# Kernel optimization log

Hardware: AMD Instinct MI355X
Metric: run time of the kernel (lower is better)

## Reference

```python
import jax, jax.numpy as jnp
import numpy as np


def setup_inputs() -> dict:
    key = jax.random.key(0)
    k1, k2, k3 = jax.random.split(key, 3)
    B, T, N = 2, 16, 128
    INP, COND, OUT = 64, 64, 128
    x = jax.random.normal(k1, (B, T, N, INP), dtype=jnp.float32)
    cond = jax.random.normal(k2, (B, N, N, COND), dtype=jnp.float32)
    in_dim = 6 * INP + 2 * COND  # 512
    W = jax.random.normal(k3, (in_dim, OUT), dtype=jnp.float32) / np.sqrt(in_dim)
    b = jnp.zeros((OUT,), dtype=jnp.float32)
    return {"x": x, "cond": cond, "W": W, "b": b}


def reference(x, cond, W, b):
    # x: (B,T,N,C), cond: (B,N,N,Cc), W: (6C+2Cc, O), b: (O,)
    B, T, N, C = x.shape
    Cc = cond.shape[-1]
    # temporal boundary-zeroed copies (faithful to torch cat of zeros + slices)
    x1 = x.at[:, 0].set(0.0)        # zeros at t=0
    x2 = x.at[:, -1].set(0.0)       # zeros at t=T-1
    xc = jnp.concatenate([x1, x, x2], axis=-1)  # (B,T,N,3C)
    # decompose the big linear over the concat [x1_pair, x2_pair, cond1, cond2]
    W1 = W[: 3 * C]
    W2 = W[3 * C: 6 * C]
    Wc1 = W[6 * C: 6 * C + Cc]
    Wc2 = W[6 * C + Cc:]
    a = jnp.einsum('btnc,co->btno', xc, W1)               # n1 contribution
    bpart = jnp.einsum('btnc,co->btno', xc, W2)            # n2 contribution
    # cond1[b,t,i,j] = cond[b,i,j]; cond2[b,t,i,j] = cond[b,j,i]
    cpart = (jnp.einsum('bijc,co->bijo', cond, Wc1)
             + jnp.einsum('bjic,co->bijo', cond, Wc2))     # (B,N,N,O)
    s = (a[:, :, :, None, :] + bpart[:, :, None, :, :]
         + cpart[:, None, :, :, :] + b)                    # (B,T,N,N,O)
    act = s * jax.nn.sigmoid(s)                            # swish
    return jnp.max(act, axis=3)                            # amax over n2 -> (B,T,N,O)
```

## Files before the change

kernel.cpp:

```cpp
#include <hip/hip_runtime.h>
#include <math.h>

#define B_ 2
#define T_ 16
#define N_ 128
#define CI 64
#define CO 128

#define AQ_OFF 0
#define BQ_OFF 524288
#define CQ_OFF 1048576
#define WF_OFF 5242880

typedef __attribute__((ext_vector_type(8))) short short8;
typedef __attribute__((ext_vector_type(4))) float f32x4;

__device__ __forceinline__ float4 f4add(float4 a, float4 b) {
  return make_float4(a.x + b.x, a.y + b.y, a.z + b.z, a.w + b.w);
}
__device__ __forceinline__ float4 f4max(float4 a, float4 b) {
  return make_float4(fmaxf(a.x, b.x), fmaxf(a.y, b.y), fmaxf(a.z, b.z), fmaxf(a.w, b.w));
}
__device__ __forceinline__ float4 f4min(float4 a, float4 b) {
  return make_float4(fminf(a.x, b.x), fminf(a.y, b.y), fminf(a.z, b.z), fminf(a.w, b.w));
}
__device__ __forceinline__ void f4fma(float4& acc, float s, float4 v) {
  acc.x = fmaf(s, v.x, acc.x);
  acc.y = fmaf(s, v.y, acc.y);
  acc.z = fmaf(s, v.z, acc.z);
  acc.w = fmaf(s, v.w, acc.w);
}
__device__ __forceinline__ float silu1(float v) { return v / (1.0f + __expf(-v)); }
__device__ __forceinline__ float4 silu4(float4 v) {
  return make_float4(silu1(v.x), silu1(v.y), silu1(v.z), silu1(v.w));
}
__device__ __forceinline__ float4 shfl4x(float4 v, int m) {
  return make_float4(__shfl_xor(v.x, m, 64), __shfl_xor(v.y, m, 64),
                     __shfl_xor(v.z, m, 64), __shfl_xor(v.w, m, 64));
}
__device__ __forceinline__ unsigned int bf2(float a, float b) {
  unsigned int ua = __float_as_uint(a);
  unsigned int ub = __float_as_uint(b);
  ua = (ua + 0x7FFFu + ((ua >> 16) & 1u)) >> 16;
  ub = (ub + 0x7FFFu + ((ub >> 16) & 1u)) >> 16;
  return (ub << 16) | ua;
}
__device__ __forceinline__ uint4 pack8(float4 lo, float4 hi) {
  return make_uint4(bf2(lo.x, lo.y), bf2(lo.z, lo.w), bf2(hi.x, hi.y), bf2(hi.z, hi.w));
}

__global__ __launch_bounds__(256) void k_prepW(const float* __restrict__ W,
                                               float* __restrict__ WF) {
  int fid = blockIdx.x * 256 + threadIdx.x;
  int lane = fid & 63;
  int ot   = (fid >> 6) & 7;
  int kh   = (fid >> 9) & 1;
  int term = fid >> 10;
  int o  = ot * 16 + (lane & 15);
  int kb = kh * 32 + (lane >> 4) * 8;
  float v[8];
  #pragma unroll
  for (int u = 0; u < 8; u++)
    v[u] = W[(384 + term * 64 + kb + u) * 128 + o];
  uint4 pk = pack8(make_float4(v[0], v[1], v[2], v[3]),
                   make_float4(v[4], v[5], v[6], v[7]));
  ((uint4*)WF)[fid] = pk;
}

__global__ __launch_bounds__(256) void k_ab2(
    const float* __restrict__ x, const float* __restrict__ W,
    const float* __restrict__ bias, float* __restrict__ AQ, float* __restrict__ BQ)
{
  __shared__ __align__(16) float WL[64 * 128];
  __shared__ float xT[64 * 17];

  int blk = blockIdx.x;
  int nq  = blk & 7;
  int dst = (blk >> 3) & 1;
  int t   = (blk >> 4) & 15;
  int b   = blk >> 8;
  float f0 = (t != 0)      ? 1.0f : 0.0f;
  float f2 = (t != T_ - 1) ? 1.0f : 0.0f;
  int tid = threadIdx.x;

  const float4* W4 = (const float4*)W;
  float4* WL4 = (float4*)WL;
  int wb = dst * 6144;
  #pragma unroll
  for (int k = 0; k < 8; k++) {
    int idx4 = tid + k * 256;
    float4 wa = W4[wb + idx4];
    float4 wm = W4[wb + 2048 + idx4];
    float4 wc = W4[wb + 4096 + idx4];
    WL4[idx4] = make_float4(f0 * wa.x + wm.x + f2 * wc.x,
                            f0 * wa.y + wm.y + f2 * wc.y,
                            f0 * wa.z + wm.z + f2 * wc.z,
                            f0 * wa.w + wm.w + f2 * wc.w);
  }
  {
    long xb = ((long)(b * T_ + t) * N_ + nq * 16) * CI;
    #pragma unroll
    for (int k = 0; k < 4; k++) {
      int idx = tid + k * 256;
      int c = idx & 63, n = idx >> 6;
      xT[c * 17 + n] = x[xb + n * CI + c];
    }
  }
  __syncthreads();

  int nl = tid & 15;
  int qg = tid >> 4;
  float4 acc0, acc1;
  if (dst == 0) {
    acc0 = ((const float4*)bias)[qg * 2];
    acc1 = ((const float4*)bias)[qg * 2 + 1];
  } else {
    acc0 = make_float4(0, 0, 0, 0); acc1 = acc0;
  }
  #pragma unroll 8
  for (int c = 0; c < 64; c++) {
    float xv = xT[c * 17 + nl];
    float4 w0 = WL4[c * 32 + qg * 2];
    float4 w1 = WL4[c * 32 + qg * 2 + 1];
    f4fma(acc0, xv, w0);
    f4fma(acc1, xv, w1);
  }
  float* dp = dst ? BQ : AQ;
  int n = nq * 16 + nl;
  long u0 = ((long)(b * 32 + qg * 2) * 16 + t) * 128 + n;
  long u1 = u0 + 16 * 128;
  ((float4*)dp)[u0] = acc0;
  ((float4*)dp)[u1] = acc1;
}

__global__ __launch_bounds__(256) void k_cp3(
    const float* __restrict__ cond, const float* __restrict__ WF,
    float* __restrict__ CQ)
{
  __shared__ __align__(16) unsigned char smem[65536];
  uint4* AF  = (uint4*)smem;
  uint4* WcF = (uint4*)(smem + 32768);
  float* Cp  = (float*)smem;

  int blk = blockIdx.x;
  int i = blk & 127;
  int b = blk >> 7;
  int tid = threadIdx.x;

  {
    const uint4* src = (const uint4*)WF;
    #pragma unroll
    for (int k = 0; k < 8; k++) WcF[tid + k * 256] = src[tid + k * 256];
  }
  #pragma unroll
  for (int term = 0; term < 2; term++) {
    #pragma unroll
    for (int k2 = 0; k2 < 4; k2++) {
      int idx = tid + k2 * 256;
      int j = idx >> 3, oct = idx & 7;
      long row = (term == 0) ? ((long)(b * N_ + i) * N_ + j)
                             : ((long)(b * N_ + j) * N_ + i);
      const float4* src = (const float4*)(cond + row * 64 + oct * 8);
      float4 lo = src[0], hi = src[1];
      int frag = ((j >> 4) * 2 + (oct >> 2)) * 64 + ((oct & 3) * 16 + (j & 15));
      AF[term * 1024 + frag] = pack8(lo, hi);
    }
  }
  __syncthreads();

  int lane = tid & 63;
  int w    = tid >> 6;
  f32x4 acc[2][8];
  #pragma unroll
  for (int jt = 0; jt < 2; jt++)
    #pragma unroll
    for (int ot = 0; ot < 8; ot++) {
      acc[jt][ot][0] = 0.f; acc[jt][ot][1] = 0.f;
      acc[jt][ot][2] = 0.f; acc[jt][ot][3] = 0.f;
    }
  const short8* AF8 = (const short8*)AF;
  const short8* WF8 = (const short8*)WcF;
  #pragma unroll
  for (int term = 0; term < 2; term++) {
    #pragma unroll
    for (int kh = 0; kh < 2; kh++) {
      short8 a0 = AF8[term * 1024 + ((2 * w + 0) * 2 + kh) * 64 + lane];
      short8 a1 = AF8[term * 1024 + ((2 * w + 1) * 2 + kh) * 64 + lane];
      #pragma unroll
      for (int ot = 0; ot < 8; ot++) {
        short8 bv = WF8[((term * 2 + kh) * 8 + ot) * 64 + lane];
        acc[0][ot] = __builtin_amdgcn_mfma_f32_16x16x32_bf16(a0, bv, acc[0][ot], 0, 0, 0);
        acc[1][ot] = __builtin_amdgcn_mfma_f32_16x16x32_bf16(a1, bv, acc[1][ot], 0, 0, 0);
      }
    }
  }
  __syncthreads();

  {
    int col = lane & 15;
    int rsub = (lane >> 4) * 4;
    #pragma unroll
    for (int jt = 0; jt < 2; jt++) {
      int row0 = (2 * w + jt) * 16 + rsub;
      #pragma unroll
      for (int ot = 0; ot < 8; ot++) {
        f32x4 d = acc[jt][ot];
        int cbase = ot * 16 + col;
        Cp[(row0 + 0) * 128 + cbase] = d[0];
        Cp[(row0 + 1) * 128 + cbase] = d[1];
        Cp[(row0 + 2) * 128 + cbase] = d[2];
        Cp[(row0 + 3) * 128 + cbase] = d[3];
      }
    }
  }
  __syncthreads();

  {
    const float4* Cp4 = (const float4*)Cp;
    float4* CQ4 = (float4*)CQ;
    #pragma unroll
    for (int it = 0; it < 16; it++) {
      int idx = tid + it * 256;
      int oq = idx & 31, j = idx >> 5;
      CQ4[((long)(b * 32 + oq) * 128 + i) * 128 + j] = Cp4[j * 32 + oq];
    }
  }
}

__global__ __launch_bounds__(256) void k_red4(
    const float* __restrict__ AQ, const float* __restrict__ BQ,
    const float* __restrict__ CQ, float* __restrict__ out)
{
  __shared__ __align__(16) float4 BpL4[128 * 9];
  __shared__ __align__(16) float4 AQL4[256];

  int blk = blockIdx.x;
  int iq = blk & 3;
  int th = (blk >> 2) & 1;
  int oq = (blk >> 3) & 31;
  int b  = blk >> 8;
  int tid = threadIdx.x;

  const float4* BQ4 = (const float4*)BQ;
  const float4* AQ4 = (const float4*)AQ;
  const float4* CQ4 = (const float4*)CQ;

  long slab4 = ((long)(b * 32 + oq) * 16 + th * 8) * 128;

  #pragma unroll
  for (int k = 0; k < 4; k++) {
    int idx = tid + k * 256;
    int t = idx >> 7, j = idx & 127;
    BpL4[j * 9 + t] = BQ4[slab4 + idx];
  }
  {
    int t = tid >> 5, il = tid & 31;
    AQL4[tid] = AQ4[slab4 + t * 128 + iq * 32 + il];
  }
  __syncthreads();

  int il = tid >> 3;
  int je = tid & 7;

  float4 mx[8], mn[8];
  #pragma unroll
  for (int t = 0; t < 8; t++) {
    mx[t] = make_float4(-3.4e38f, -3.4e38f, -3.4e38f, -3.4e38f);
    mn[t] = make_float4(3.4e38f, 3.4e38f, 3.4e38f, 3.4e38f);
  }

  const float4* CQr = CQ4 + ((long)(b * 32 + oq) * 128 + iq * 32 + il) * 128 + je;

  #pragma unroll
  for (int jj = 0; jj < 16; jj += 4) {
    float4 c0 = CQr[(jj + 0) * 8];
    float4 c1 = CQr[(jj + 1) * 8];
    float4 c2 = CQr[(jj + 2) * 8];
    float4 c3 = CQr[(jj + 3) * 8];
    int jb0 = (je + 8 * (jj + 0)) * 9;
    int jb1 = (je + 8 * (jj + 1)) * 9;
    int jb2 = (je + 8 * (jj + 2)) * 9;
    int jb3 = (je + 8 * (jj + 3)) * 9;
    #pragma unroll
    for (int t = 0; t < 8; t++) {
      float4 s0 = f4add(c0, BpL4[jb0 + t]);
      float4 s1 = f4add(c1, BpL4[jb1 + t]);
      float4 s2 = f4add(c2, BpL4[jb2 + t]);
      float4 s3 = f4add(c3, BpL4[jb3 + t]);
      mx[t] = f4max(mx[t], f4max(f4max(s0, s1), f4max(s2, s3)));
      mn[t] = f4min(mn[t], f4min(f4min(s0, s1), f4min(s2, s3)));
    }
  }

  #pragma unroll
  for (int t = 0; t < 8; t++) {
    mx[t] = f4max(mx[t], shfl4x(mx[t], 1));
    mn[t] = f4min(mn[t], shfl4x(mn[t], 1));
    mx[t] = f4max(mx[t], shfl4x(mx[t], 2));
    mn[t] = f4min(mn[t], shfl4x(mn[t], 2));
    mx[t] = f4max(mx[t], shfl4x(mx[t], 4));
    mn[t] = f4min(mn[t], shfl4x(mn[t], 4));
  }

  if (je == 0) {
    int i = iq * 32 + il;
    #pragma unroll
    for (int t = 0; t < 8; t++) {
      float4 av = AQL4[t * 32 + il];
      float4 M  = f4add(mx[t], av);
      float4 Mn = f4add(mn[t], av);
      float4 res = f4max(silu4(M), silu4(Mn));
      ((float4*)out)[(long)((b * 16 + th * 8 + t) * 128 + i) * 32 + oq] = res;
    }
  }
}

extern "C" void kernel_launch(void* const* d_in, const int* in_sizes, int n_in,
                              void* d_out, int out_size, void* d_ws, size_t ws_size,
                              hipStream_t stream) {
  const float* x    = (const float*)d_in[0];
  const float* cond = (const float*)d_in[1];
  const float* W    = (const float*)d_in[2];
  const float* bias = (const float*)d_in[3];
  float* out = (float*)d_out;

  float* ws = (float*)d_ws;
  float* AQ = ws + AQ_OFF;
  float* BQ = ws + BQ_OFF;
  float* CQ = ws + CQ_OFF;
  float* WF = ws + WF_OFF;

  k_prepW<<<8, 256, 0, stream>>>(W, WF);
  k_ab2<<<512, 256, 0, stream>>>(x, W, bias, AQ, BQ);
  k_cp3<<<256, 256, 0, stream>>>(cond, WF, CQ);
  k_red4<<<512, 256, 0, stream>>>(AQ, BQ, CQ, out);
}
```

Baseline: 109.5 us.

## Split cond GEMM over j halves and simplify reduction to per-thread loops

The cond projection kernel now splits each i row into two j halves, doubling the grid to 512 blocks and cutting shared memory, with a padded stride-132 staging buffer to reduce bank conflicts on the transpose. The reduction kernel drops shared-memory staging and warp shuffles: each thread owns one (t,i) pair and loops over all 128 j, reading CQ and BQ directly from global/L2. This trades cross-lane reduction and LDS traffic for more redundant global loads of BQ and longer per-thread loops.

```diff
diff --git a/kernel.cpp b/kernel.cpp
--- a/kernel.cpp
+++ b/kernel.cpp
@@ -33,10 +33,6 @@
 __device__ __forceinline__ float silu1(float v) { return v / (1.0f + __expf(-v)); }
 __device__ __forceinline__ float4 silu4(float4 v) {
   return make_float4(silu1(v.x), silu1(v.y), silu1(v.z), silu1(v.w));
-}
-__device__ __forceinline__ float4 shfl4x(float4 v, int m) {
-  return make_float4(__shfl_xor(v.x, m, 64), __shfl_xor(v.y, m, 64),
-                     __shfl_xor(v.z, m, 64), __shfl_xor(v.w, m, 64));
 }
 __device__ __forceinline__ unsigned int bf2(float a, float b) {
   unsigned int ua = __float_as_uint(a);
@@ -62,9 +58,8 @@
   #pragma unroll
   for (int u = 0; u < 8; u++)
     v[u] = W[(384 + term * 64 + kb + u) * 128 + o];
-  uint4 pk = pack8(make_float4(v[0], v[1], v[2], v[3]),
-                   make_float4(v[4], v[5], v[6], v[7]));
-  ((uint4*)WF)[fid] = pk;
+  ((uint4*)WF)[fid] = pack8(make_float4(v[0], v[1], v[2], v[3]),
+                            make_float4(v[4], v[5], v[6], v[7]));
 }
 
 __global__ __launch_bounds__(256) void k_ab2(
@@ -133,18 +128,19 @@
   ((float4*)dp)[u1] = acc1;
 }
 
-__global__ __launch_bounds__(256) void k_cp3(
+__global__ __launch_bounds__(256) void k_cp4(
     const float* __restrict__ cond, const float* __restrict__ WF,
     float* __restrict__ CQ)
 {
-  __shared__ __align__(16) unsigned char smem[65536];
+  __shared__ __align__(16) unsigned char smem[49152];
   uint4* AF  = (uint4*)smem;
-  uint4* WcF = (uint4*)(smem + 32768);
+  uint4* WcF = (uint4*)(smem + 16384);
   float* Cp  = (float*)smem;
 
   int blk = blockIdx.x;
-  int i = blk & 127;
-  int b = blk >> 7;
+  int jh = blk & 1;
+  int i  = (blk >> 1) & 127;
+  int b  = blk >> 8;
   int tid = threadIdx.x;
 
   {
@@ -153,44 +149,38 @@
     for (int k = 0; k < 8; k++) WcF[tid + k * 256] = src[tid + k * 256];
   }
   #pragma unroll
-  for (int term = 0; term < 2; term++) {
-    #pragma unroll
-    for (int k2 = 0; k2 < 4; k2++) {
-      int idx = tid + k2 * 256;
-      int j = idx >> 3, oct = idx & 7;
-      long row = (term == 0) ? ((long)(b * N_ + i) * N_ + j)
-                             : ((long)(b * N_ + j) * N_ + i);
-      const float4* src = (const float4*)(cond + row * 64 + oct * 8);
-      float4 lo = src[0], hi = src[1];
-      int frag = ((j >> 4) * 2 + (oct >> 2)) * 64 + ((oct & 3) * 16 + (j & 15));
-      AF[term * 1024 + frag] = pack8(lo, hi);
-    }
+  for (int k = 0; k < 4; k++) {
+    int idx = tid + k * 256;
+    int term = idx >> 9;
+    int rem = idx & 511;
+    int jl = rem >> 3, oct = rem & 7;
+    long row = (term == 0) ? ((long)(b * N_ + i) * N_ + jh * 64 + jl)
+                           : ((long)(b * N_ + jh * 64 + jl) * N_ + i);
+    const float4* src = (const float4*)(cond + row * 64 + oct * 8);
+    float4 lo = src[0], hi = src[1];
+    int frag = term * 512 + ((jl >> 4) * 2 + (oct >> 2)) * 64 + (oct & 3) * 16 + (jl & 15);
+    AF[frag] = pack8(lo, hi);
   }
   __syncthreads();
 
   int lane = tid & 63;
   int w    = tid >> 6;
-  f32x4 acc[2][8];
-  #pragma unroll
-  for (int jt = 0; jt < 2; jt++)
-    #pragma unroll
-    for (int ot = 0; ot < 8; ot++) {
-      acc[jt][ot][0] = 0.f; acc[jt][ot][1] = 0.f;
-      acc[jt][ot][2] = 0.f; acc[jt][ot][3] = 0.f;
-    }
+  f32x4 acc[8];
+  #pragma unroll
+  for (int ot = 0; ot < 8; ot++) {
+    acc[ot][0] = 0.f; acc[ot][1] = 0.f; acc[ot][2] = 0.f; acc[ot][3] = 0.f;
+  }
   const short8* AF8 = (const short8*)AF;
   const short8* WF8 = (const short8*)WcF;
   #pragma unroll
   for (int term = 0; term < 2; term++) {
     #pragma unroll
     for (int kh = 0; kh < 2; kh++) {
-      short8 a0 = AF8[term * 1024 + ((2 * w + 0) * 2 + kh) * 64 + lane];
-      short8 a1 = AF8[term * 1024 + ((2 * w + 1) * 2 + kh) * 64 + lane];
+      short8 a = AF8[term * 512 + (w * 2 + kh) * 64 + lane];
       #pragma unroll
       for (int ot = 0; ot < 8; ot++) {
         short8 bv = WF8[((term * 2 + kh) * 8 + ot) * 64 + lane];
-        acc[0][ot] = __builtin_amdgcn_mfma_f32_16x16x32_bf16(a0, bv, acc[0][ot], 0, 0, 0);
-        acc[1][ot] = __builtin_amdgcn_mfma_f32_16x16x32_bf16(a1, bv, acc[1][ot], 0, 0, 0);
+        acc[ot] = __builtin_amdgcn_mfma_f32_16x16x32_bf16(a, bv, acc[ot], 0, 0, 0);
       }
     }
   }
@@ -198,19 +188,15 @@
 
   {
     int col = lane & 15;
-    int rsub = (lane >> 4) * 4;
-    #pragma unroll
-    for (int jt = 0; jt < 2; jt++) {
-      int row0 = (2 * w + jt) * 16 + rsub;
-      #pragma unroll
-      for (int ot = 0; ot < 8; ot++) {
-        f32x4 d = acc[jt][ot];
-        int cbase = ot * 16 + col;
-        Cp[(row0 + 0) * 128 + cbase] = d[0];
-        Cp[(row0 + 1) * 128 + cbase] = d[1];
-        Cp[(row0 + 2) * 128 + cbase] = d[2];
-        Cp[(row0 + 3) * 128 + cbase] = d[3];
-      }
+    int row0 = w * 16 + (lane >> 4) * 4;
+    #pragma unroll
+    for (int ot = 0; ot < 8; ot++) {
+      f32x4 d = acc[ot];
+      int cbase = ot * 16 + col;
+      Cp[(row0 + 0) * 132 + cbase] = d[0];
+      Cp[(row0 + 1) * 132 + cbase] = d[1];
+      Cp[(row0 + 2) * 132 + cbase] = d[2];
+      Cp[(row0 + 3) * 132 + cbase] = d[3];
     }
   }
   __syncthreads();
@@ -219,100 +205,52 @@
     const float4* Cp4 = (const float4*)Cp;
     float4* CQ4 = (float4*)CQ;
     #pragma unroll
-    for (int it = 0; it < 16; it++) {
+    for (int it = 0; it < 8; it++) {
       int idx = tid + it * 256;
-      int oq = idx & 31, j = idx >> 5;
-      CQ4[((long)(b * 32 + oq) * 128 + i) * 128 + j] = Cp4[j * 32 + oq];
-    }
-  }
-}
-
-__global__ __launch_bounds__(256) void k_red4(
+      int oq = idx >> 6, jl = idx & 63;
+      CQ4[((long)(b * 32 + oq) * 128 + i) * 128 + jh * 64 + jl] = Cp4[jl * 33 + oq];
+    }
+  }
+}
+
+__global__ __launch_bounds__(256) void k_red6(
     const float* __restrict__ AQ, const float* __restrict__ BQ,
     const float* __restrict__ CQ, float* __restrict__ out)
 {
-  __shared__ __align__(16) float4 BpL4[128 * 9];
-  __shared__ __align__(16) float4 AQL4[256];
-
   int blk = blockIdx.x;
   int iq = blk & 3;
   int th = (blk >> 2) & 1;
   int oq = (blk >> 3) & 31;
   int b  = blk >> 8;
   int tid = threadIdx.x;
-
-  const float4* BQ4 = (const float4*)BQ;
-  const float4* AQ4 = (const float4*)AQ;
-  const float4* CQ4 = (const float4*)CQ;
-
-  long slab4 = ((long)(b * 32 + oq) * 16 + th * 8) * 128;
-
-  #pragma unroll
-  for (int k = 0; k < 4; k++) {
-    int idx = tid + k * 256;
-    int t = idx >> 7, j = idx & 127;
-    BpL4[j * 9 + t] = BQ4[slab4 + idx];
-  }
-  {
-    int t = tid >> 5, il = tid & 31;
-    AQL4[tid] = AQ4[slab4 + t * 128 + iq * 32 + il];
-  }
-  __syncthreads();
-
-  int il = tid >> 3;
-  int je = tid & 7;
-
-  float4 mx[8], mn[8];
-  #pragma unroll
-  for (int t = 0; t < 8; t++) {
-    mx[t] = make_float4(-3.4e38f, -3.4e38f, -3.4e38f, -3.4e38f);
-    mn[t] = make_float4(3.4e38f, 3.4e38f, 3.4e38f, 3.4e38f);
-  }
-
-  const float4* CQr = CQ4 + ((long)(b * 32 + oq) * 128 + iq * 32 + il) * 128 + je;
-
-  #pragma unroll
-  for (int jj = 0; jj < 16; jj += 4) {
-    float4 c0 = CQr[(jj + 0) * 8];
-    float4 c1 = CQr[(jj + 1) * 8];
-    float4 c2 = CQr[(jj + 2) * 8];
-    float4 c3 = CQr[(jj + 3) * 8];
-    int jb0 = (je + 8 * (jj + 0)) * 9;
-    int jb1 = (je + 8 * (jj + 1)) * 9;
-    int jb2 = (je + 8 * (jj + 2)) * 9;
-    int jb3 = (je + 8 * (jj + 3)) * 9;
-    #pragma unroll
-    for (int t = 0; t < 8; t++) {
-      float4 s0 = f4add(c0, BpL4[jb0 + t]);
-      float4 s1 = f4add(c1, BpL4[jb1 + t]);
-      float4 s2 = f4add(c2, BpL4[jb2 + t]);
-      float4 s3 = f4add(c3, BpL4[jb3 + t]);
-      mx[t] = f4max(mx[t], f4max(f4max(s0, s1), f4max(s2, s3)));
-      mn[t] = f4min(mn[t], f4min(f4min(s0, s1), f4min(s2, s3)));
-    }
-  }
-
-  #pragma unroll
-  for (int t = 0; t < 8; t++) {
-    mx[t] = f4max(mx[t], shfl4x(mx[t], 1));
-    mn[t] = f4min(mn[t], shfl4x(mn[t], 1));
-    mx[t] = f4max(mx[t], shfl4x(mx[t], 2));
-    mn[t] = f4min(mn[t], shfl4x(mn[t], 2));
-    mx[t] = f4max(mx[t], shfl4x(mx[t], 4));
-    mn[t] = f4min(mn[t], shfl4x(mn[t], 4));
-  }
-
-  if (je == 0) {
-    int i = iq * 32 + il;
-    #pragma unroll
-    for (int t = 0; t < 8; t++) {
-      float4 av = AQL4[t * 32 + il];
-      float4 M  = f4add(mx[t], av);
-      float4 Mn = f4add(mn[t], av);
-      float4 res = f4max(silu4(M), silu4(Mn));
-      ((float4*)out)[(long)((b * 16 + th * 8 + t) * 128 + i) * 32 + oq] = res;
-    }
-  }
+  int w    = tid >> 6;
+  int lane = tid & 63;
+  int t = th * 8 + (lane >> 3);
+  int i = iq * 32 + w * 8 + (lane & 7);
+
+  const float4* CQr = (const float4*)CQ + ((long)(b * 32 + oq) * 128 + i) * 128;
+  const float4* BQr = (const float4*)BQ + ((long)(b * 32 + oq) * 16 + t) * 128;
+
+  float4 mx0 = make_float4(-3.4e38f, -3.4e38f, -3.4e38f, -3.4e38f);
+  float4 mx1 = mx0;
+  float4 mn0 = make_float4(3.4e38f, 3.4e38f, 3.4e38f, 3.4e38f);
+  float4 mn1 = mn0;
+
+  #pragma unroll 4
+  for (int j = 0; j < 128; j += 2) {
+    float4 s0 = f4add(CQr[j],     BQr[j]);
+    float4 s1 = f4add(CQr[j + 1], BQr[j + 1]);
+    mx0 = f4max(mx0, s0); mn0 = f4min(mn0, s0);
+    mx1 = f4max(mx1, s1); mn1 = f4min(mn1, s1);
+  }
+  float4 mx = f4max(mx0, mx1);
+  float4 mn = f4min(mn0, mn1);
+
+  float4 av = ((const float4*)AQ)[((long)(b * 32 + oq) * 16 + t) * 128 + i];
+  float4 M  = f4add(mx, av);
+  float4 Mn = f4add(mn, av);
+  float4 res = f4max(silu4(M), silu4(Mn));
+  ((float4*)out)[(long)((b * 16 + t) * 128 + i) * 32 + oq] = res;
 }
 
 extern "C" void kernel_launch(void* const* d_in, const int* in_sizes, int n_in,
@@ -332,6 +270,6 @@
 
   k_prepW<<<8, 256, 0, stream>>>(W, WF);
   k_ab2<<<512, 256, 0, stream>>>(x, W, bias, AQ, BQ);
-  k_cp3<<<256, 256, 0, stream>>>(cond, WF, CQ);
-  k_red4<<<512, 256, 0, stream>>>(AQ, BQ, CQ, out);
-}
+  k_cp4<<<512, 256, 0, stream>>>(cond, WF, CQ);
+  k_red6<<<512, 256, 0, stream>>>(AQ, BQ, CQ, out);
+}
```

After: 122.9 us. 1.12x slower.

## Fuse cond projection with max-reduction and fold W packing into fused kernel

Applied to the files above, without the earlier changes.

Removes the separate W-prep and reduction kernels. The cond-projection kernel now packs the W slice to bf16 in-block and then directly performs the max/min-over-j reduction from its LDS tile, with B written in a transposed layout so it can be read coalesced. This avoids writing and re-reading the large CQ intermediate and cuts two launches. In exchange, each of only 256 blocks redundantly converts W, and the reduction is done by fewer blocks, each reading all of BT for every t.

```diff
diff --git a/kernel.cpp b/kernel.cpp
--- a/kernel.cpp
+++ b/kernel.cpp
@@ -8,9 +8,7 @@
 #define CO 128
 
 #define AQ_OFF 0
-#define BQ_OFF 524288
-#define CQ_OFF 1048576
-#define WF_OFF 5242880
+#define BT_OFF 524288
 
 typedef __attribute__((ext_vector_type(8))) short short8;
 typedef __attribute__((ext_vector_type(4))) float f32x4;
@@ -49,27 +47,9 @@
   return make_uint4(bf2(lo.x, lo.y), bf2(lo.z, lo.w), bf2(hi.x, hi.y), bf2(hi.z, hi.w));
 }
 
-__global__ __launch_bounds__(256) void k_prepW(const float* __restrict__ W,
-                                               float* __restrict__ WF) {
-  int fid = blockIdx.x * 256 + threadIdx.x;
-  int lane = fid & 63;
-  int ot   = (fid >> 6) & 7;
-  int kh   = (fid >> 9) & 1;
-  int term = fid >> 10;
-  int o  = ot * 16 + (lane & 15);
-  int kb = kh * 32 + (lane >> 4) * 8;
-  float v[8];
-  #pragma unroll
-  for (int u = 0; u < 8; u++)
-    v[u] = W[(384 + term * 64 + kb + u) * 128 + o];
-  uint4 pk = pack8(make_float4(v[0], v[1], v[2], v[3]),
-                   make_float4(v[4], v[5], v[6], v[7]));
-  ((uint4*)WF)[fid] = pk;
-}
-
-__global__ __launch_bounds__(256) void k_ab2(
+__global__ __launch_bounds__(256) void k_ab3(
     const float* __restrict__ x, const float* __restrict__ W,
-    const float* __restrict__ bias, float* __restrict__ AQ, float* __restrict__ BQ)
+    const float* __restrict__ bias, float* __restrict__ AQ, float* __restrict__ BT)
 {
   __shared__ __align__(16) float WL[64 * 128];
   __shared__ float xT[64 * 17];
@@ -125,17 +105,22 @@
     f4fma(acc0, xv, w0);
     f4fma(acc1, xv, w1);
   }
-  float* dp = dst ? BQ : AQ;
   int n = nq * 16 + nl;
-  long u0 = ((long)(b * 32 + qg * 2) * 16 + t) * 128 + n;
-  long u1 = u0 + 16 * 128;
-  ((float4*)dp)[u0] = acc0;
-  ((float4*)dp)[u1] = acc1;
-}
-
-__global__ __launch_bounds__(256) void k_cp3(
-    const float* __restrict__ cond, const float* __restrict__ WF,
-    float* __restrict__ CQ)
+  if (dst == 0) {
+    long u0 = ((long)(b * 32 + qg * 2) * 16 + t) * 128 + n;
+    ((float4*)AQ)[u0]            = acc0;
+    ((float4*)AQ)[u0 + 16 * 128] = acc1;
+  } else {
+    long u0 = (((long)(b * 16 + t) * 128) + n) * 32 + qg * 2;
+    ((float4*)BT)[u0]     = acc0;
+    ((float4*)BT)[u0 + 1] = acc1;
+  }
+}
+
+__global__ __launch_bounds__(256) void k_fused(
+    const float* __restrict__ cond, const float* __restrict__ W,
+    const float* __restrict__ AQ, const float* __restrict__ BT,
+    float* __restrict__ out)
 {
   __shared__ __align__(16) unsigned char smem[65536];
   uint4* AF  = (uint4*)smem;
@@ -147,10 +132,21 @@
   int b = blk >> 7;
   int tid = threadIdx.x;
 
-  {
-    const uint4* src = (const uint4*)WF;
-    #pragma unroll
-    for (int k = 0; k < 8; k++) WcF[tid + k * 256] = src[tid + k * 256];
+  #pragma unroll
+  for (int f = 0; f < 8; f++) {
+    int fid = tid + f * 256;
+    int lane_f = fid & 63;
+    int ot   = (fid >> 6) & 7;
+    int kh   = (fid >> 9) & 1;
+    int term = fid >> 10;
+    int o  = ot * 16 + (lane_f & 15);
+    int kb = kh * 32 + (lane_f >> 4) * 8;
+    float v[8];
+    #pragma unroll
+    for (int u = 0; u < 8; u++)
+      v[u] = W[(384 + term * 64 + kb + u) * 128 + o];
+    WcF[fid] = pack8(make_float4(v[0], v[1], v[2], v[3]),
+                     make_float4(v[4], v[5], v[6], v[7]));
   }
   #pragma unroll
   for (int term = 0; term < 2; term++) {
@@ -215,102 +211,39 @@
   }
   __syncthreads();
 
-  {
-    const float4* Cp4 = (const float4*)Cp;
-    float4* CQ4 = (float4*)CQ;
-    #pragma unroll
-    for (int it = 0; it < 16; it++) {
-      int idx = tid + it * 256;
-      int oq = idx & 31, j = idx >> 5;
-      CQ4[((long)(b * 32 + oq) * 128 + i) * 128 + j] = Cp4[j * 32 + oq];
-    }
-  }
-}
-
-__global__ __launch_bounds__(256) void k_red4(
-    const float* __restrict__ AQ, const float* __restrict__ BQ,
-    const float* __restrict__ CQ, float* __restrict__ out)
-{
-  __shared__ __align__(16) float4 BpL4[128 * 9];
-  __shared__ __align__(16) float4 AQL4[256];
-
-  int blk = blockIdx.x;
-  int iq = blk & 3;
-  int th = (blk >> 2) & 1;
-  int oq = (blk >> 3) & 31;
-  int b  = blk >> 8;
-  int tid = threadIdx.x;
-
-  const float4* BQ4 = (const float4*)BQ;
+  int jh = lane >> 5;
+  int oq = lane & 31;
+  const float4* Cp4 = (const float4*)Cp;
   const float4* AQ4 = (const float4*)AQ;
-  const float4* CQ4 = (const float4*)CQ;
-
-  long slab4 = ((long)(b * 32 + oq) * 16 + th * 8) * 128;
-
-  #pragma unroll
-  for (int k = 0; k < 4; k++) {
-    int idx = tid + k * 256;
-    int t = idx >> 7, j = idx & 127;
-    BpL4[j * 9 + t] = BQ4[slab4 + idx];
-  }
-  {
-    int t = tid >> 5, il = tid & 31;
-    AQL4[tid] = AQ4[slab4 + t * 128 + iq * 32 + il];
-  }
-  __syncthreads();
-
-  int il = tid >> 3;
-  int je = tid & 7;
-
-  float4 mx[8], mn[8];
-  #pragma unroll
-  for (int t = 0; t < 8; t++) {
-    mx[t] = make_float4(-3.4e38f, -3.4e38f, -3.4e38f, -3.4e38f);
-    mn[t] = make_float4(3.4e38f, 3.4e38f, 3.4e38f, 3.4e38f);
-  }
-
-  const float4* CQr = CQ4 + ((long)(b * 32 + oq) * 128 + iq * 32 + il) * 128 + je;
-
-  #pragma unroll
-  for (int jj = 0; jj < 16; jj += 4) {
-    float4 c0 = CQr[(jj + 0) * 8];
-    float4 c1 = CQr[(jj + 1) * 8];
-    float4 c2 = CQr[(jj + 2) * 8];
-    float4 c3 = CQr[(jj + 3) * 8];
-    int jb0 = (je + 8 * (jj + 0)) * 9;
-    int jb1 = (je + 8 * (jj + 1)) * 9;
-    int jb2 = (je + 8 * (jj + 2)) * 9;
-    int jb3 = (je + 8 * (jj + 3)) * 9;
-    #pragma unroll
-    for (int t = 0; t < 8; t++) {
-      float4 s0 = f4add(c0, BpL4[jb0 + t]);
-      float4 s1 = f4add(c1, BpL4[jb1 + t]);
-      float4 s2 = f4add(c2, BpL4[jb2 + t]);
-      float4 s3 = f4add(c3, BpL4[jb3 + t]);
-      mx[t] = f4max(mx[t], f4max(f4max(s0, s1), f4max(s2, s3)));
-      mn[t] = f4min(mn[t], f4min(f4min(s0, s1), f4min(s2, s3)));
-    }
-  }
-
-  #pragma unroll
-  for (int t = 0; t < 8; t++) {
-    mx[t] = f4max(mx[t], shfl4x(mx[t], 1));
-    mn[t] = f4min(mn[t], shfl4x(mn[t], 1));
-    mx[t] = f4max(mx[t], shfl4x(mx[t], 2));
-    mn[t] = f4min(mn[t], shfl4x(mn[t], 2));
-    mx[t] = f4max(mx[t], shfl4x(mx[t], 4));
-    mn[t] = f4min(mn[t], shfl4x(mn[t], 4));
-  }
-
-  if (je == 0) {
-    int i = iq * 32 + il;
-    #pragma unroll
-    for (int t = 0; t < 8; t++) {
-      float4 av = AQL4[t * 32 + il];
-      float4 M  = f4add(mx[t], av);
-      float4 Mn = f4add(mn[t], av);
+  const float4* BT4 = (const float4*)BT;
+
+  #pragma unroll
+  for (int tt = 0; tt < 4; tt++) {
+    int t = w * 4 + tt;
+    const float4* bq = BT4 + ((long)(b * 16 + t) * 128) * 32;
+    float4 mx = make_float4(-3.4e38f, -3.4e38f, -3.4e38f, -3.4e38f);
+    float4 mn = make_float4(3.4e38f, 3.4e38f, 3.4e38f, 3.4e38f);
+    #pragma unroll
+    for (int jj = 0; jj < 64; jj += 8) {
+      float4 s[8];
+      #pragma unroll
+      for (int k = 0; k < 8; k++)
+        s[k] = bq[(jh * 64 + jj + k) * 32 + oq];
+      #pragma unroll
+      for (int k = 0; k < 8; k++) {
+        float4 v = f4add(s[k], Cp4[(jh * 64 + jj + k) * 32 + oq]);
+        mx = f4max(mx, v);
+        mn = f4min(mn, v);
+      }
+    }
+    mx = f4max(mx, shfl4x(mx, 32));
+    mn = f4min(mn, shfl4x(mn, 32));
+    if (jh == 0) {
+      float4 av = AQ4[((long)(b * 32 + oq) * 16 + t) * 128 + i];
+      float4 M  = f4add(mx, av);
+      float4 Mn = f4add(mn, av);
       float4 res = f4max(silu4(M), silu4(Mn));
-      ((float4*)out)[(long)((b * 16 + th * 8 + t) * 128 + i) * 32 + oq] = res;
+      ((float4*)out)[(long)((b * 16 + t) * 128 + i) * 32 + oq] = res;
     }
   }
 }
@@ -326,12 +259,8 @@
 
   float* ws = (float*)d_ws;
   float* AQ = ws + AQ_OFF;
-  float* BQ = ws + BQ_OFF;
-  float* CQ = ws + CQ_OFF;
-  float* WF = ws + WF_OFF;
-
-  k_prepW<<<8, 256, 0, stream>>>(W, WF);
-  k_ab2<<<512, 256, 0, stream>>>(x, W, bias, AQ, BQ);
-  k_cp3<<<256, 256, 0, stream>>>(cond, WF, CQ);
-  k_red4<<<512, 256, 0, stream>>>(AQ, BQ, CQ, out);
-}
+  float* BT = ws + BT_OFF;
+
+  k_ab3<<<512, 256, 0, stream>>>(x, W, bias, AQ, BT);
+  k_fused<<<256, 256, 0, stream>>>(cond, W, AQ, BT, out);
+}
```

After: 93.45 us. 14.7% less time.
